# Kernel optimization log

Hardware: AMD Instinct MI355X
Metric: run time of the kernel (lower is better)

Reference implementation:

```python
import jax, jax.numpy as jnp
import numpy as np

HIDDEN = 1024
HEADS = 16
HEAD = HIDDEN // HEADS
EXPAND = 4096
EPS = 1e-5


def layer_norm(x, g, b):
    mu = jnp.mean(x, axis=-1, keepdims=True)
    var = jnp.mean((x - mu) ** 2, axis=-1, keepdims=True)
    return (x - mu) * jax.lax.rsqrt(var + EPS) * g + b


def setup_inputs() -> dict:
    key = jax.random.key(0)
    ks = jax.random.split(key, 12)
    s = 0.02
    return {
        "x": jax.random.normal(ks[0], (4, 2048, HIDDEN), dtype=jnp.float32),
        "Wqkv": jax.random.normal(ks[1], (HIDDEN, 3 * HIDDEN), dtype=jnp.float32) * s,
        "bqkv": jnp.zeros((3 * HIDDEN,), jnp.float32),
        "Wproj": jax.random.normal(ks[2], (HIDDEN, HIDDEN), dtype=jnp.float32) * s,
        "bproj": jnp.zeros((HIDDEN,), jnp.float32),
        "W1": jax.random.normal(ks[3], (HIDDEN, EXPAND), dtype=jnp.float32) * s,
        "b1": jnp.zeros((EXPAND,), jnp.float32),
        "W2": jax.random.normal(ks[4], (EXPAND, HIDDEN), dtype=jnp.float32) * s,
        "b2": jnp.zeros((HIDDEN,), jnp.float32),
        "g1": jnp.ones((HIDDEN,), jnp.float32),
        "be1": jnp.zeros((HIDDEN,), jnp.float32),
        "g2": jnp.ones((HIDDEN,), jnp.float32),
        "be2": jnp.zeros((HIDDEN,), jnp.float32),
    }


def attention(x, Wqkv, bqkv, Wproj, bproj):
    B, L, _ = x.shape
    qkv = (x @ Wqkv + bqkv).reshape(B, L, 3, HEADS, HEAD)
    q, k, v = [qkv[:, :, i].transpose(0, 2, 1, 3) for i in range(3)]  # [B,H,L,D]
    attn = jnp.einsum("bnld,bnkd->bnlk", q, k) / np.sqrt(HEAD).astype(np.float32)
    attn = jax.nn.softmax(attn, axis=-1)
    o = jnp.einsum("bnlk,bnkd->bnld", attn, v)
    o = o.transpose(0, 2, 1, 3).reshape(B, L, HIDDEN)
    return o @ Wproj + bproj


def reference(x, Wqkv, bqkv, Wproj, bproj, W1, b1, W2, b2, g1, be1, g2, be2):
    # post-norm transformer block (pre_norm=False), dropout=0 (eval)
    h = layer_norm(x + attention(x, Wqkv, bqkv, Wproj, bproj), g1, be1)
    ff = jax.nn.gelu(h @ W1 + b1, approximate=False) @ W2 + b2
    return layer_norm(h + ff, g2, be2)
```

## Files before the change

### kernel.cpp

```cpp
#include <hip/hip_runtime.h>
#include <hip/hip_bf16.h>
#include <math.h>


typedef __bf16 bf16_t;
typedef __bf16 bf16x8 __attribute__((ext_vector_type(8)));
typedef __bf16 bf16x4 __attribute__((ext_vector_type(4)));
typedef float f32x4 __attribute__((ext_vector_type(4)));
typedef float f32x16 __attribute__((ext_vector_type(16)));

#define HID   1024
#define NHEAD 16
#define HD    64
#define EXPD  4096
#define LSEQ  2048
#define BATCH 4
#define MROWS (BATCH * LSEQ)

#if __has_builtin(__builtin_amdgcn_exp2f)
#define EXP2F __builtin_amdgcn_exp2f
#else
#define EXP2F exp2f
#endif

__device__ __forceinline__ void gld_lds16(const bf16_t* g, bf16_t* l) {
  __builtin_amdgcn_global_load_lds(
      (const __attribute__((address_space(1))) void*)g,
      (__attribute__((address_space(3))) void*)l, 16, 0, 0);
}

__device__ __forceinline__ void vmwait(int n) {
  if (n == 8)      asm volatile("s_waitcnt vmcnt(8)" ::: "memory");
  else if (n == 4) asm volatile("s_waitcnt vmcnt(4)" ::: "memory");
  else if (n == 3) asm volatile("s_waitcnt vmcnt(3)" ::: "memory");
  else if (n == 0) asm volatile("s_waitcnt vmcnt(0)" ::: "memory");
}

__device__ __forceinline__ void block_bar() {
  asm volatile("" ::: "memory");
  __builtin_amdgcn_s_barrier();
  asm volatile("" ::: "memory");
}

__device__ __forceinline__ void swap32(unsigned& a, unsigned& b) {
#if __has_builtin(__builtin_amdgcn_permlane32_swap)
  auto r = __builtin_amdgcn_permlane32_swap(a, b, false, false);
  a = r[0]; b = r[1];
#else
  bool hiL = ((threadIdx.x & 63) >= 32);
  unsigned pa = (unsigned)__shfl_xor((int)a, 32, 64);
  unsigned pb = (unsigned)__shfl_xor((int)b, 32, 64);
  unsigned na = hiL ? pb : a;
  unsigned nb = hiL ? b : pa;
  a = na; b = nb;
#endif
}

__device__ __forceinline__ unsigned pk_bf16(float lo, float hi) {
  bf16_t l = (bf16_t)lo, h = (bf16_t)hi;
  unsigned short ul, uh;
  __builtin_memcpy(&ul, &l, 2);
  __builtin_memcpy(&uh, &h, 2);
  return (unsigned)ul | ((unsigned)uh << 16);
}

__device__ __forceinline__ float gelu_t(float v) {
  float u = v * (0.7978845608028654f + 0.0356774081f * v * v);
  float e = EXP2F(u * 2.885390082f);
  float th = (e - 1.f) / (e + 1.f);
  return 0.5f * v * (1.f + th);
}

__global__ __launch_bounds__(256) void cvt_bf16(const float* __restrict__ in,
                                                bf16_t* __restrict__ out, int n4) {
  int i = blockIdx.x * 256 + threadIdx.x;
  if (i >= n4) return;
  float4 v = ((const float4*)in)[i];
  bf16x4 o;
  o[0] = (bf16_t)v.x; o[1] = (bf16_t)v.y; o[2] = (bf16_t)v.z; o[3] = (bf16_t)v.w;
  ((bf16x4*)out)[i] = o;
}

__global__ __launch_bounds__(256) void transpose_cvt(const float* __restrict__ W,
                                                     bf16_t* __restrict__ Wt,
                                                     int K, int N) {
  __shared__ float tile[32][33];
  int n0 = blockIdx.x * 32, k0 = blockIdx.y * 32;
  int tx = threadIdx.x & 31, ty = threadIdx.x >> 5;
#pragma unroll
  for (int i = 0; i < 32; i += 8)
    tile[ty + i][tx] = W[(size_t)(k0 + ty + i) * N + n0 + tx];
  __syncthreads();
#pragma unroll
  for (int i = 0; i < 32; i += 8)
    Wt[(size_t)(n0 + ty + i) * K + k0 + tx] = (bf16_t)tile[tx][ty + i];
}

template <int BM, int BN, int NTHR>
__global__ __launch_bounds__(NTHR, (NTHR == 512 ? 4 : 3))
void gemm_k(const bf16_t* __restrict__ A,
            const bf16_t* __restrict__ Bt,
            const float* __restrict__ bias,
            void* __restrict__ C,
            float* __restrict__ C2,
            bf16_t* __restrict__ vTo,
            int M, int N, int K, int mode) {
  constexpr int WC = (NTHR / 64) / 2;
  constexpr int AL = BM * 4 / NTHR;
  constexpr int BL = BN * 4 / NTHR;
  constexpr int LOADS = AL + BL;
  constexpr int RSTEP = NTHR >> 2;
  __shared__ bf16_t smem[3 * BM * 32 + 3 * BN * 32];
  bf16_t* As = smem;
  bf16_t* Bs = smem + 3 * BM * 32;

  const int nbx = gridDim.x;
  int p = blockIdx.y * nbx + blockIdx.x;
  const int GM = 8;
  int group = p / (GM * nbx);
  int idx = p - group * (GM * nbx);
  const int by = group * GM + (idx & (GM - 1));
  const int bx = idx >> 3;
  const int n0 = bx * BN, m0 = by * BM;

  const int zz = blockIdx.z;
  const int kLen = K / (int)gridDim.z;
  const int kOff = zz * kLen;

  const int t = threadIdx.x;
  const int lane = t & 63, w = t >> 6;
  const int wr = w / WC, wc = w % WC;
  const int quad = lane >> 4, l16 = lane & 15;

  f32x4 acc[4][4];
#pragma unroll
  for (int i = 0; i < 4; ++i)
#pragma unroll
    for (int j = 0; j < 4; ++j) acc[i][j] = (f32x4){0.f, 0.f, 0.f, 0.f};

  const int r0 = t >> 2;
  const unsigned ksw = (((unsigned)t & 3u) ^ ((unsigned)(r0 >> 1) & 3u)) * 8u;
  const unsigned offR0 = (unsigned)r0 * (unsigned)K + ksw;

  const bf16_t* aB = A + (size_t)m0 * K + kOff;
  const bf16_t* bB = Bt + (size_t)n0 * K + kOff;

  unsigned aoff[4], boff[4];
#pragma unroll
  for (int i = 0; i < 4; ++i) {
    int row = wr * 64 + 16 * i + l16;
    aoff[i] = (unsigned)(row * 32 + (quad ^ ((row >> 1) & 3)) * 8);
  }
#pragma unroll
  for (int j = 0; j < 4; ++j) {
    int row = wc * 64 + 16 * j + l16;
    boff[j] = (unsigned)(row * 32 + (quad ^ ((row >> 1) & 3)) * 8);
  }

  auto stage = [&](int slot, int kk) {
    bf16_t* Asl = As + slot * (BM * 32);
    bf16_t* Bsl = Bs + slot * (BN * 32);
    const bf16_t* aS = aB + kk;
    const bf16_t* bS = bB + kk;
#pragma unroll
    for (int a = 0; a < AL; ++a)
      gld_lds16(aS + offR0 + (size_t)a * RSTEP * K, Asl + (t + a * NTHR) * 8);
#pragma unroll
    for (int b = 0; b < BL; ++b)
      gld_lds16(bS + offR0 + (size_t)b * RSTEP * K, Bsl + (t + b * NTHR) * 8);
  };

  const int NT = kLen >> 5;

  stage(0, 0);
  stage(1, 32);
  vmwait(LOADS);
  block_bar();

  int cs = 0;
  for (int kt = 0; kt < NT; ++kt) {
    if (kt < NT - 2) {
      int ss = cs == 0 ? 2 : cs - 1;
      stage(ss, (kt + 2) * 32);
    }
    const bf16_t* Asl = As + cs * (BM * 32);
    const bf16_t* Bsl = Bs + cs * (BN * 32);
    bf16x8 af[4], bfr[4];
#pragma unroll
    for (int i = 0; i < 4; ++i) af[i] = *(const bf16x8*)(Asl + aoff[i]);
#pragma unroll
    for (int j = 0; j < 4; ++j) bfr[j] = *(const bf16x8*)(Bsl + boff[j]);
    __builtin_amdgcn_s_setprio(1);
#pragma unroll
    for (int i = 0; i < 4; ++i)
#pragma unroll
      for (int j = 0; j < 4; ++j)
        acc[i][j] = __builtin_amdgcn_mfma_f32_16x16x32_bf16(af[i], bfr[j], acc[i][j], 0, 0, 0);
    __builtin_amdgcn_s_setprio(0);
    if (kt < NT - 2)      vmwait(LOADS);
    else if (kt == NT - 2) vmwait(0);
    if (kt < NT - 1) block_bar();
    cs = cs == 2 ? 0 : cs + 1;
  }

  if constexpr (BN == 256) {
    if (vTo != nullptr && n0 >= 2048) {
      const int bb = m0 >> 11;
      const int l0b = m0 & 2047;
      block_bar();
      bf16_t* T = smem;
#pragma unroll
      for (int i = 0; i < 4; ++i) {
        int rl = wr * 64 + 16 * i + quad * 4;
#pragma unroll
        for (int j = 0; j < 4; ++j) {
          int c = wc * 64 + 16 * j + l16;
          float bv = bias[n0 + c];
          bf16x4 pk;
#pragma unroll
          for (int r = 0; r < 4; ++r) pk[r] = (bf16_t)(acc[i][j][r] + bv);
          *(bf16x4*)(T + c * 132 + rl) = pk;
        }
      }
      block_bar();
      const int vbase = n0 - 2048;
#pragma unroll
      for (int s = 0; s < 4096 / NTHR; ++s) {
        int id = t + s * NTHR;
        int c = id >> 4, ch = id & 15;
        int hh = (vbase + c) >> 6, dd = (vbase + c) & 63;
        bf16x8 v8 = *(const bf16x8*)(T + c * 132 + ch * 8);
        *(bf16x8*)(vTo + ((size_t)((bb * 16 + hh) * 64 + dd)) * 2048 + l0b + ch * 8) = v8;
      }
      return;
    }
  }

#pragma unroll
  for (int i = 0; i < 4; ++i) {
    int rowb = m0 + wr * 64 + 16 * i + quad * 4;
#pragma unroll
    for (int j = 0; j < 4; ++j) {
      int col = n0 + wc * 64 + 16 * j + l16;
      float bv = (zz == 0) ? bias[col] : 0.f;
#pragma unroll
      for (int r = 0; r < 4; ++r) {
        float v = acc[i][j][r] + bv;
        size_t idx = (size_t)(rowb + r) * N + col;
        if (zz != 0) {
          C2[idx] = v;
        } else if (mode == 0) {
          ((bf16_t*)C)[idx] = (bf16_t)v;
        } else if (mode == 1) {
          ((bf16_t*)C)[idx] = (bf16_t)gelu_t(v);
        } else {
          ((float*)C)[idx] = v;
        }
      }
    }
  }
}

__global__ __launch_bounds__(512, 2)
void gemm_8x(const bf16_t* __restrict__ A,
             const bf16_t* __restrict__ Bt,
             const float* __restrict__ bias,
             bf16_t* __restrict__ C,
             int M, int N, int K) {
  __shared__ bf16_t smem[65536];
  const int nbx = gridDim.x;
  int p = blockIdx.y * nbx + blockIdx.x;
  const int GM = 8;
  int group = p / (GM * nbx);
  int idx = p - group * (GM * nbx);
  const int by = group * GM + (idx & (GM - 1));
  const int bx = idx >> 3;
  const int n0 = bx * 256, m0 = by * 256;

  const int t = threadIdx.x;
  const int lane = t & 63, w = t >> 6;
  const int wr = w >> 2, wc = w & 3;
  const int quad = lane >> 4, l16 = lane & 15;

  f32x4 acc[8][4];
#pragma unroll
  for (int i = 0; i < 8; ++i)
#pragma unroll
    for (int j = 0; j < 4; ++j) acc[i][j] = (f32x4){0.f, 0.f, 0.f, 0.f};

  const int r0 = t >> 2;
  const unsigned ksw = (((unsigned)t & 3u) ^ ((unsigned)(r0 >> 1) & 3u)) * 8u;
  const unsigned offR = (unsigned)r0 * (unsigned)K + ksw;

  const bf16_t* aB = A + (size_t)m0 * K;
  const bf16_t* bB = Bt + (size_t)n0 * K;

  unsigned aoff[8], boff[4];
#pragma unroll
  for (int i = 0; i < 8; ++i) {
    int row = wr * 128 + 16 * i + l16;
    aoff[i] = (unsigned)(row * 32 + (quad ^ ((row >> 1) & 3)) * 8);
  }
#pragma unroll
  for (int j = 0; j < 4; ++j) {
    int row = wc * 64 + 16 * j + l16;
    boff[j] = (unsigned)(16384 + row * 32 + (quad ^ ((row >> 1) & 3)) * 8);
  }

  auto stageChunk = [&](const bf16_t* src, int kk, int regionElem) {
    bf16_t* d = smem + regionElem;
    gld_lds16(src + kk + offR, d + t * 8);
    gld_lds16(src + kk + offR + (size_t)128 * K, d + t * 8 + 4096);
  };

  const int NT = K >> 6;

  stageChunk(aB, 0, 0);
  stageChunk(bB, 0, 16384);
  stageChunk(aB, 32, 8192);
  stageChunk(bB, 32, 24576);
  vmwait(4);
  block_bar();

  for (int kt = 0; kt < NT; ++kt) {
    const int sb = (kt & 1) * 32768;
    const int ss = ((kt + 1) & 1) * 32768;
    const int ktk = (kt + 1) * 64;
    const bool st = (kt + 1 < NT);
    bf16x8 af[8], b0, b1;
#pragma unroll
    for (int i = 0; i < 8; ++i) af[i] = *(const bf16x8*)(smem + sb + aoff[i]);
    b0 = *(const bf16x8*)(smem + sb + boff[0]);
    b1 = *(const bf16x8*)(smem + sb + boff[1]);
    if (st) stageChunk(aB, ktk, ss);
    __builtin_amdgcn_s_setprio(1);
#pragma unroll
    for (int i = 0; i < 8; ++i) {
      acc[i][0] = __builtin_amdgcn_mfma_f32_16x16x32_bf16(af[i], b0, acc[i][0], 0, 0, 0);
      acc[i][1] = __builtin_amdgcn_mfma_f32_16x16x32_bf16(af[i], b1, acc[i][1], 0, 0, 0);
    }
    __builtin_amdgcn_s_setprio(0);
    b0 = *(const bf16x8*)(smem + sb + boff[2]);
    b1 = *(const bf16x8*)(smem + sb + boff[3]);
    if (st) stageChunk(bB, ktk, ss + 16384);
    __builtin_amdgcn_s_setprio(1);
#pragma unroll
    for (int i = 0; i < 8; ++i) {
      acc[i][2] = __builtin_amdgcn_mfma_f32_16x16x32_bf16(af[i], b0, acc[i][2], 0, 0, 0);
      acc[i][3] = __builtin_amdgcn_mfma_f32_16x16x32_bf16(af[i], b1, acc[i][3], 0, 0, 0);
    }
    __builtin_amdgcn_s_setprio(0);
    if (st) vmwait(4); else vmwait(0);
    block_bar();
#pragma unroll
    for (int i = 0; i < 8; ++i) af[i] = *(const bf16x8*)(smem + sb + 8192 + aoff[i]);
    b0 = *(const bf16x8*)(smem + sb + 8192 + boff[0]);
    b1 = *(const bf16x8*)(smem + sb + 8192 + boff[1]);
    if (st) stageChunk(aB, ktk + 32, ss + 8192);
    __builtin_amdgcn_s_setprio(1);
#pragma unroll
    for (int i = 0; i < 8; ++i) {
      acc[i][0] = __builtin_amdgcn_mfma_f32_16x16x32_bf16(af[i], b0, acc[i][0], 0, 0, 0);
      acc[i][1] = __builtin_amdgcn_mfma_f32_16x16x32_bf16(af[i], b1, acc[i][1], 0, 0, 0);
    }
    __builtin_amdgcn_s_setprio(0);
    b0 = *(const bf16x8*)(smem + sb + 8192 + boff[2]);
    b1 = *(const bf16x8*)(smem + sb + 8192 + boff[3]);
    if (st) stageChunk(bB, ktk + 32, ss + 24576);
    __builtin_amdgcn_s_setprio(1);
#pragma unroll
    for (int i = 0; i < 8; ++i) {
      acc[i][2] = __builtin_amdgcn_mfma_f32_16x16x32_bf16(af[i], b0, acc[i][2], 0, 0, 0);
      acc[i][3] = __builtin_amdgcn_mfma_f32_16x16x32_bf16(af[i], b1, acc[i][3], 0, 0, 0);
    }
    __builtin_amdgcn_s_setprio(0);
    if (st) {
      vmwait(4);
      block_bar();
    }
  }

#pragma unroll
  for (int i = 0; i < 8; ++i) {
    int rowb = m0 + wr * 128 + 16 * i + quad * 4;
#pragma unroll
    for (int j = 0; j < 4; ++j) {
      int col = n0 + wc * 64 + 16 * j + l16;
      float bv = bias[col];
#pragma unroll
      for (int r = 0; r < 4; ++r) {
        float v = acc[i][j][r] + bv;
        C[(size_t)(rowb + r) * N + col] = (bf16_t)gelu_t(v);
      }
    }
  }
}

__global__ __launch_bounds__(256, 3) void attn_kernel(const bf16_t* __restrict__ qkv,
                                                      const bf16_t* __restrict__ vT,
                                                      bf16_t* __restrict__ ob) {
  __shared__ bf16_t smem[24576];
  bf16_t* Qs = smem + 16384;
  const int qt = blockIdx.x, h = blockIdx.y, b = blockIdx.z;
  const int t = threadIdx.x, lane = t & 63, w = t >> 6;
  const int l32 = lane & 31, hi = lane >> 5;
  const size_t RS = 3 * HID;
  const int bh = b * NHEAD + h;

  const bf16_t* qbase = qkv + ((size_t)(b * LSEQ + qt * 128)) * RS + h * HD;
  const bf16_t* kbase = qkv + ((size_t)b * LSEQ) * RS + HID + h * HD;
  const bf16_t* vtbase = vT + (size_t)bh * HD * LSEQ;

#pragma unroll
  for (int s = 0; s < 4; ++s) {
    int l = t + s * 256;
    int r = l >> 3, c8 = l & 7;
    gld_lds16(qbase + (size_t)r * RS + ((c8 ^ (r & 7)) * 8), Qs + l * 8);
  }
  __syncthreads();

  const float sc = 0.18033688011112042f;
  bf16x8 bq[4];
  {
    int qrow = 32 * w + l32;
#pragma unroll
    for (int c = 0; c < 4; ++c) {
      int y = 2 * c + hi;
      bf16x8 q8 = *(const bf16x8*)(Qs + qrow * 64 + ((y ^ (qrow & 7)) * 8));
#pragma unroll
      for (int e = 0; e < 8; ++e) q8[e] = (bf16_t)((float)q8[e] * sc);
      bq[c] = q8;
    }
  }

  bf16x8 ones8;
#pragma unroll
  for (int e = 0; e < 8; ++e) ones8[e] = (bf16_t)1.0f;

  auto stageKV = [&](int slot, int kt) {
    bf16_t* Ks = smem + slot * 8192;
    bf16_t* Vts = Ks + 4096;
#pragma unroll
    for (int s = 0; s < 2; ++s) {
      int l = t + s * 256;
      int r = l >> 3, c8 = l & 7;
      gld_lds16(kbase + (size_t)(kt * 64 + r) * RS + ((c8 ^ (r & 7)) * 8), Ks + l * 8);
      gld_lds16(vtbase + (size_t)r * LSEQ + kt * 64 + ((c8 ^ (r & 7)) * 8), Vts + l * 8);
    }
  };

  f32x16 accO[2], accS;
#pragma unroll
  for (int dt = 0; dt < 2; ++dt)
#pragma unroll
    for (int e = 0; e < 16; ++e) accO[dt][e] = 0.f;
#pragma unroll
  for (int e = 0; e < 16; ++e) accS[e] = 0.f;

  constexpr int NT = LSEQ / 64;
  stageKV(0, 0);

  for (int kt = 0; kt < NT; ++kt) {
    const int cs = kt & 1;
    if (kt + 1 < NT) {
      stageKV(1 - cs, kt + 1);
      vmwait(4);
    } else {
      vmwait(0);
    }
    block_bar();
    const bf16_t* Ks = smem + cs * 8192;
    const bf16_t* Vts = Ks + 4096;

    f32x16 s0, s1;
#pragma unroll
    for (int e = 0; e < 16; ++e) { s0[e] = 0.f; s1[e] = 0.f; }
    __builtin_amdgcn_s_setprio(1);
#pragma unroll
    for (int c = 0; c < 4; ++c) {
      int y = 2 * c + hi;
      int r0 = l32;
      bf16x8 a0 = *(const bf16x8*)(Ks + r0 * 64 + ((y ^ (r0 & 7)) * 8));
      s0 = __builtin_amdgcn_mfma_f32_32x32x16_bf16(a0, bq[c], s0, 0, 0, 0);
      int r1 = 32 + l32;
      bf16x8 a1 = *(const bf16x8*)(Ks + r1 * 64 + ((y ^ (r1 & 7)) * 8));
      s1 = __builtin_amdgcn_mfma_f32_32x32x16_bf16(a1, bq[c], s1, 0, 0, 0);
    }
    __builtin_amdgcn_s_setprio(0);

    unsigned pf[2][2][4];
#pragma unroll
    for (int stile = 0; stile < 2; ++stile) {
      f32x16& sv = stile ? s1 : s0;
      float p[16];
#pragma unroll
      for (int e = 0; e < 16; ++e) p[e] = EXP2F(sv[e]);
      unsigned lo[4], hi_[4];
#pragma unroll
      for (int g = 0; g < 4; ++g) {
        lo[g] = pk_bf16(p[4 * g + 0], p[4 * g + 1]);
        hi_[g] = pk_bf16(p[4 * g + 2], p[4 * g + 3]);
      }
#pragma unroll
      for (int c2 = 0; c2 < 2; ++c2) {
        unsigned aL = lo[2 * c2], bL = lo[2 * c2 + 1];
        swap32(aL, bL);
        pf[stile][c2][0] = aL; pf[stile][c2][2] = bL;
        unsigned aH = hi_[2 * c2], bH = hi_[2 * c2 + 1];
        swap32(aH, bH);
        pf[stile][c2][1] = aH; pf[stile][c2][3] = bH;
      }
    }

    __builtin_amdgcn_s_setprio(1);
#pragma unroll
    for (int dt = 0; dt < 2; ++dt)
#pragma unroll
      for (int stile = 0; stile < 2; ++stile)
#pragma unroll
        for (int c2 = 0; c2 < 2; ++c2) {
          int c8v = stile * 4 + c2 * 2 + hi;
          int rv = dt * 32 + l32;
          bf16x8 av = *(const bf16x8*)(Vts + rv * 64 + ((c8v ^ (rv & 7)) * 8));
          union { unsigned u[4]; bf16x8 v; } bp;
          bp.u[0] = pf[stile][c2][0]; bp.u[1] = pf[stile][c2][1];
          bp.u[2] = pf[stile][c2][2]; bp.u[3] = pf[stile][c2][3];
          accO[dt] = __builtin_amdgcn_mfma_f32_32x32x16_bf16(av, bp.v, accO[dt], 0, 0, 0);
        }
#pragma unroll
    for (int stile = 0; stile < 2; ++stile)
#pragma unroll
      for (int c2 = 0; c2 < 2; ++c2) {
        union { unsigned u[4]; bf16x8 v; } bp;
        bp.u[0] = pf[stile][c2][0]; bp.u[1] = pf[stile][c2][1];
        bp.u[2] = pf[stile][c2][2]; bp.u[3] = pf[stile][c2][3];
        accS = __builtin_amdgcn_mfma_f32_32x32x16_bf16(ones8, bp.v, accS, 0, 0, 0);
      }
    __builtin_amdgcn_s_setprio(0);
    block_bar();
  }

  float inv = 1.f / accS[0];

  bf16_t* Osh = smem;
  {
    int q = 32 * w + l32;
#pragma unroll
    for (int dt = 0; dt < 2; ++dt)
#pragma unroll
      for (int e = 0; e < 16; ++e) {
        int d = dt * 32 + (e & 3) + 8 * (e >> 2) + 4 * hi;
        Osh[q * 68 + d] = (bf16_t)(accO[dt][e] * inv);
      }
  }
  __syncthreads();
#pragma unroll
  for (int s = 0; s < 4; ++s) {
    int l = t + s * 256;
    int r = l >> 3, c8 = l & 7;
    bf16x8 v = *(const bf16x8*)(Osh + r * 68 + c8 * 8);
    *(bf16x8*)(ob + ((size_t)(b * LSEQ + qt * 128 + r)) * HID + h * HD + c8 * 8) = v;
  }
}

__global__ __launch_bounds__(256) void resid_ln(const float* __restrict__ X,
                                                const float* __restrict__ Y,
                                                const float* __restrict__ Y2,
                                                const float* __restrict__ g,
                                                const float* __restrict__ be,
                                                float* __restrict__ outf,
                                                bf16_t* __restrict__ outb) {
  const int row = blockIdx.x;
  const int t = threadIdx.x;
  float4 a = ((const float4*)X)[(size_t)row * 256 + t];
  float4 bvec = ((const float4*)Y)[(size_t)row * 256 + t];
  float4 cvec = {0.f, 0.f, 0.f, 0.f};
  if (Y2) cvec = ((const float4*)Y2)[(size_t)row * 256 + t];
  float v0 = a.x + bvec.x + cvec.x, v1 = a.y + bvec.y + cvec.y;
  float v2 = a.z + bvec.z + cvec.z, v3 = a.w + bvec.w + cvec.w;
  float s = v0 + v1 + v2 + v3;
  float s2 = v0 * v0 + v1 * v1 + v2 * v2 + v3 * v3;
#pragma unroll
  for (int msk = 1; msk < 64; msk <<= 1) {
    s += __shfl_xor(s, msk, 64);
    s2 += __shfl_xor(s2, msk, 64);
  }
  __shared__ float red[8];
  int w = t >> 6;
  if ((t & 63) == 0) { red[w] = s; red[w + 4] = s2; }
  __syncthreads();
  s = red[0] + red[1] + red[2] + red[3];
  s2 = red[4] + red[5] + red[6] + red[7];
  float mu = s * (1.f / 1024.f);
  float var = s2 * (1.f / 1024.f) - mu * mu;
  float rstd = rsqrtf(var + 1e-5f);
  float4 gg = ((const float4*)g)[t];
  float4 bb = ((const float4*)be)[t];
  float o0 = (v0 - mu) * rstd * gg.x + bb.x;
  float o1 = (v1 - mu) * rstd * gg.y + bb.y;
  float o2 = (v2 - mu) * rstd * gg.z + bb.z;
  float o3 = (v3 - mu) * rstd * gg.w + bb.w;
  float4 o = {o0, o1, o2, o3};
  ((float4*)outf)[(size_t)row * 256 + t] = o;
  if (outb) {
    bf16x4 ob4;
    ob4[0] = (bf16_t)o0; ob4[1] = (bf16_t)o1; ob4[2] = (bf16_t)o2; ob4[3] = (bf16_t)o3;
    ((bf16x4*)outb)[(size_t)row * 256 + t] = ob4;
  }
}

extern "C" void kernel_launch(void* const* d_in, const int* in_sizes, int n_in,
                              void* d_out, int out_size, void* d_ws, size_t ws_size,
                              hipStream_t stream) {
  const float* x     = (const float*)d_in[0];
  const float* Wqkv  = (const float*)d_in[1];
  const float* bqkv  = (const float*)d_in[2];
  const float* Wproj = (const float*)d_in[3];
  const float* bproj = (const float*)d_in[4];
  const float* W1    = (const float*)d_in[5];
  const float* b1    = (const float*)d_in[6];
  const float* W2    = (const float*)d_in[7];
  const float* b2    = (const float*)d_in[8];
  const float* g1    = (const float*)d_in[9];
  const float* be1   = (const float*)d_in[10];
  const float* g2    = (const float*)d_in[11];
  const float* be2   = (const float*)d_in[12];
  float* out = (float*)d_out;

  char* ws = (char*)d_ws;
  bf16_t* w2T    = (bf16_t*)(ws);
  float*  h      = (float*) (ws + ((size_t)8 << 20));
  float*  a_f2   = (float*) (ws + ((size_t)40 << 20));
  bf16_t* qkv_ff = (bf16_t*)(ws + ((size_t)72 << 20));
  char*   E      = ws + ((size_t)136 << 20);
  bf16_t* wqkvT  = (bf16_t*)(E);
  bf16_t* wprojT = (bf16_t*)(E + ((size_t)6 << 20));
  bf16_t* w1T    = (bf16_t*)(E + ((size_t)8 << 20));
  char*   xb_ob  = E + ((size_t)16 << 20);
  bf16_t* hb     = (bf16_t*)(E + ((size_t)32 << 20));
  float*  f2b    = (float*)E;

  bf16_t* xb    = (bf16_t*)xb_ob;
  bf16_t* ob    = (bf16_t*)xb_ob;
  bf16_t* qkvb  = qkv_ff;
  bf16_t* ff1b  = qkv_ff;
  float*  attnf = a_f2;
  float*  ff2f  = a_f2;
  bf16_t* vTg   = hb;

  dim3 blk(256);
  dim3 blk512(512);
  transpose_cvt<<<dim3(3072 / 32, 1024 / 32), blk, 0, stream>>>(Wqkv, wqkvT, 1024, 3072);
  transpose_cvt<<<dim3(1024 / 32, 1024 / 32), blk, 0, stream>>>(Wproj, wprojT, 1024, 1024);
  transpose_cvt<<<dim3(4096 / 32, 1024 / 32), blk, 0, stream>>>(W1, w1T, 1024, 4096);
  transpose_cvt<<<dim3(1024 / 32, 4096 / 32), blk, 0, stream>>>(W2, w2T, 4096, 1024);
  cvt_bf16<<<MROWS * HID / 4 / 256, blk, 0, stream>>>(x, xb, MROWS * HID / 4);

  gemm_k<128, 256, 512><<<dim3(3072 / 256, MROWS / 128), blk512, 0, stream>>>(
      xb, wqkvT, bqkv, qkvb, nullptr, vTg, MROWS, 3072, 1024, 0);
  attn_kernel<<<dim3(LSEQ / 128, NHEAD, BATCH), blk, 0, stream>>>(qkvb, vTg, ob);
  gemm_k<128, 256, 512><<<dim3(1024 / 256, MROWS / 128, 2), blk512, 0, stream>>>(
      ob, wprojT, bproj, attnf, h, nullptr, MROWS, 1024, 1024, 2);
  resid_ln<<<MROWS, blk, 0, stream>>>(x, attnf, h, g1, be1, h, hb);
  gemm_8x<<<dim3(4096 / 256, MROWS / 256), blk512, 0, stream>>>(
      hb, w1T, b1, ff1b, MROWS, 4096, 1024);
  gemm_k<128, 256, 512><<<dim3(1024 / 256, MROWS / 128, 2), blk512, 0, stream>>>(
      ff1b, w2T, b2, ff2f, f2b, nullptr, MROWS, 1024, 4096, 2);
  resid_ln<<<MROWS, blk, 0, stream>>>(h, ff2f, f2b, g2, be2, out, (bf16_t*)nullptr);
}
```

Before: 532.0 us.

## Double attention query tile per block to reuse K/V tiles across more queries

The attention kernel now processes 256 query rows per block instead of 128, with each wave handling two 32-row query sub-tiles. Each K/V tile staged in shared memory and each K/V fragment read from LDS is reused for twice as many MFMAs, which halves global K/V traffic and the barrier count per query. In exchange it uses more registers and LDS, drops occupancy to 2 blocks per CU, and halves the grid to 512 blocks.

```diff
diff --git a/kernel.cpp b/kernel.cpp
--- a/kernel.cpp
+++ b/kernel.cpp
@@ -396,10 +396,10 @@
   }
 }
 
-__global__ __launch_bounds__(256, 3) void attn_kernel(const bf16_t* __restrict__ qkv,
+__global__ __launch_bounds__(256, 2) void attn_kernel(const bf16_t* __restrict__ qkv,
                                                       const bf16_t* __restrict__ vT,
                                                       bf16_t* __restrict__ ob) {
-  __shared__ bf16_t smem[24576];
+  __shared__ bf16_t smem[32768];
   bf16_t* Qs = smem + 16384;
   const int qt = blockIdx.x, h = blockIdx.y, b = blockIdx.z;
   const int t = threadIdx.x, lane = t & 63, w = t >> 6;
@@ -407,12 +407,12 @@
   const size_t RS = 3 * HID;
   const int bh = b * NHEAD + h;
 
-  const bf16_t* qbase = qkv + ((size_t)(b * LSEQ + qt * 128)) * RS + h * HD;
+  const bf16_t* qbase = qkv + ((size_t)(b * LSEQ + qt * 256)) * RS + h * HD;
   const bf16_t* kbase = qkv + ((size_t)b * LSEQ) * RS + HID + h * HD;
   const bf16_t* vtbase = vT + (size_t)bh * HD * LSEQ;
 
 #pragma unroll
-  for (int s = 0; s < 4; ++s) {
+  for (int s = 0; s < 8; ++s) {
     int l = t + s * 256;
     int r = l >> 3, c8 = l & 7;
     gld_lds16(qbase + (size_t)r * RS + ((c8 ^ (r & 7)) * 8), Qs + l * 8);
@@ -420,16 +420,21 @@
   __syncthreads();
 
   const float sc = 0.18033688011112042f;
-  bf16x8 bq[4];
+  bf16x8 bqA[4], bqB[4];
   {
-    int qrow = 32 * w + l32;
+    int qA = 64 * w + l32, qB = qA + 32;
 #pragma unroll
     for (int c = 0; c < 4; ++c) {
       int y = 2 * c + hi;
-      bf16x8 q8 = *(const bf16x8*)(Qs + qrow * 64 + ((y ^ (qrow & 7)) * 8));
-#pragma unroll
-      for (int e = 0; e < 8; ++e) q8[e] = (bf16_t)((float)q8[e] * sc);
-      bq[c] = q8;
+      bf16x8 qa = *(const bf16x8*)(Qs + qA * 64 + ((y ^ (qA & 7)) * 8));
+      bf16x8 qb = *(const bf16x8*)(Qs + qB * 64 + ((y ^ (qB & 7)) * 8));
+#pragma unroll
+      for (int e = 0; e < 8; ++e) {
+        qa[e] = (bf16_t)((float)qa[e] * sc);
+        qb[e] = (bf16_t)((float)qb[e] * sc);
+      }
+      bqA[c] = qa;
+      bqB[c] = qb;
     }
   }
 
@@ -449,13 +454,13 @@
     }
   };
 
-  f32x16 accO[2], accS;
-#pragma unroll
-  for (int dt = 0; dt < 2; ++dt)
-#pragma unroll
-    for (int e = 0; e < 16; ++e) accO[dt][e] = 0.f;
-#pragma unroll
-  for (int e = 0; e < 16; ++e) accS[e] = 0.f;
+  f32x16 accOA[2], accOB[2], accSA, accSB, z16;
+#pragma unroll
+  for (int e = 0; e < 16; ++e) {
+    accOA[0][e] = 0.f; accOA[1][e] = 0.f;
+    accOB[0][e] = 0.f; accOB[1][e] = 0.f;
+    accSA[e] = 0.f; accSB[e] = 0.f; z16[e] = 0.f;
+  }
 
   constexpr int NT = LSEQ / 64;
   stageKV(0, 0);
@@ -472,45 +477,58 @@
     const bf16_t* Ks = smem + cs * 8192;
     const bf16_t* Vts = Ks + 4096;
 
-    f32x16 s0, s1;
-#pragma unroll
-    for (int e = 0; e < 16; ++e) { s0[e] = 0.f; s1[e] = 0.f; }
+    f32x16 sA0, sA1, sB0, sB1;
     __builtin_amdgcn_s_setprio(1);
-#pragma unroll
-    for (int c = 0; c < 4; ++c) {
+    {
+      int y = hi;
+      int r0 = l32, r1 = 32 + l32;
+      bf16x8 a0 = *(const bf16x8*)(Ks + r0 * 64 + ((y ^ (r0 & 7)) * 8));
+      bf16x8 a1 = *(const bf16x8*)(Ks + r1 * 64 + ((y ^ (r1 & 7)) * 8));
+      sA0 = __builtin_amdgcn_mfma_f32_32x32x16_bf16(a0, bqA[0], z16, 0, 0, 0);
+      sA1 = __builtin_amdgcn_mfma_f32_32x32x16_bf16(a1, bqA[0], z16, 0, 0, 0);
+      sB0 = __builtin_amdgcn_mfma_f32_32x32x16_bf16(a0, bqB[0], z16, 0, 0, 0);
+      sB1 = __builtin_amdgcn_mfma_f32_32x32x16_bf16(a1, bqB[0], z16, 0, 0, 0);
+    }
+#pragma unroll
+    for (int c = 1; c < 4; ++c) {
       int y = 2 * c + hi;
-      int r0 = l32;
+      int r0 = l32, r1 = 32 + l32;
       bf16x8 a0 = *(const bf16x8*)(Ks + r0 * 64 + ((y ^ (r0 & 7)) * 8));
-      s0 = __builtin_amdgcn_mfma_f32_32x32x16_bf16(a0, bq[c], s0, 0, 0, 0);
-      int r1 = 32 + l32;
       bf16x8 a1 = *(const bf16x8*)(Ks + r1 * 64 + ((y ^ (r1 & 7)) * 8));
-      s1 = __builtin_amdgcn_mfma_f32_32x32x16_bf16(a1, bq[c], s1, 0, 0, 0);
+      sA0 = __builtin_amdgcn_mfma_f32_32x32x16_bf16(a0, bqA[c], sA0, 0, 0, 0);
+      sA1 = __builtin_amdgcn_mfma_f32_32x32x16_bf16(a1, bqA[c], sA1, 0, 0, 0);
+      sB0 = __builtin_amdgcn_mfma_f32_32x32x16_bf16(a0, bqB[c], sB0, 0, 0, 0);
+      sB1 = __builtin_amdgcn_mfma_f32_32x32x16_bf16(a1, bqB[c], sB1, 0, 0, 0);
     }
     __builtin_amdgcn_s_setprio(0);
 
-    unsigned pf[2][2][4];
-#pragma unroll
-    for (int stile = 0; stile < 2; ++stile) {
-      f32x16& sv = stile ? s1 : s0;
-      float p[16];
-#pragma unroll
-      for (int e = 0; e < 16; ++e) p[e] = EXP2F(sv[e]);
-      unsigned lo[4], hi_[4];
-#pragma unroll
-      for (int g = 0; g < 4; ++g) {
-        lo[g] = pk_bf16(p[4 * g + 0], p[4 * g + 1]);
-        hi_[g] = pk_bf16(p[4 * g + 2], p[4 * g + 3]);
-      }
-#pragma unroll
-      for (int c2 = 0; c2 < 2; ++c2) {
-        unsigned aL = lo[2 * c2], bL = lo[2 * c2 + 1];
-        swap32(aL, bL);
-        pf[stile][c2][0] = aL; pf[stile][c2][2] = bL;
-        unsigned aH = hi_[2 * c2], bH = hi_[2 * c2 + 1];
-        swap32(aH, bH);
-        pf[stile][c2][1] = aH; pf[stile][c2][3] = bH;
-      }
-    }
+    unsigned pfA[2][2][4], pfB[2][2][4];
+    auto mkpf = [&](f32x16& s0, f32x16& s1, unsigned (&pf)[2][2][4]) {
+#pragma unroll
+      for (int stile = 0; stile < 2; ++stile) {
+        f32x16& sv = stile ? s1 : s0;
+        float p[16];
+#pragma unroll
+        for (int e = 0; e < 16; ++e) p[e] = EXP2F(sv[e]);
+        unsigned lo[4], hi_[4];
+#pragma unroll
+        for (int g = 0; g < 4; ++g) {
+          lo[g] = pk_bf16(p[4 * g + 0], p[4 * g + 1]);
+          hi_[g] = pk_bf16(p[4 * g + 2], p[4 * g + 3]);
+        }
+#pragma unroll
+        for (int c2 = 0; c2 < 2; ++c2) {
+          unsigned aL = lo[2 * c2], bL = lo[2 * c2 + 1];
+          swap32(aL, bL);
+          pf[stile][c2][0] = aL; pf[stile][c2][2] = bL;
+          unsigned aH = hi_[2 * c2], bH = hi_[2 * c2 + 1];
+          swap32(aH, bH);
+          pf[stile][c2][1] = aH; pf[stile][c2][3] = bH;
+        }
+      }
+    };
+    mkpf(sA0, sA1, pfA);
+    mkpf(sB0, sB1, pfB);
 
     __builtin_amdgcn_s_setprio(1);
 #pragma unroll
@@ -522,44 +540,52 @@
           int c8v = stile * 4 + c2 * 2 + hi;
           int rv = dt * 32 + l32;
           bf16x8 av = *(const bf16x8*)(Vts + rv * 64 + ((c8v ^ (rv & 7)) * 8));
-          union { unsigned u[4]; bf16x8 v; } bp;
-          bp.u[0] = pf[stile][c2][0]; bp.u[1] = pf[stile][c2][1];
-          bp.u[2] = pf[stile][c2][2]; bp.u[3] = pf[stile][c2][3];
-          accO[dt] = __builtin_amdgcn_mfma_f32_32x32x16_bf16(av, bp.v, accO[dt], 0, 0, 0);
+          union { unsigned u[4]; bf16x8 v; } ba, bb;
+          ba.u[0] = pfA[stile][c2][0]; ba.u[1] = pfA[stile][c2][1];
+          ba.u[2] = pfA[stile][c2][2]; ba.u[3] = pfA[stile][c2][3];
+          bb.u[0] = pfB[stile][c2][0]; bb.u[1] = pfB[stile][c2][1];
+          bb.u[2] = pfB[stile][c2][2]; bb.u[3] = pfB[stile][c2][3];
+          accOA[dt] = __builtin_amdgcn_mfma_f32_32x32x16_bf16(av, ba.v, accOA[dt], 0, 0, 0);
+          accOB[dt] = __builtin_amdgcn_mfma_f32_32x32x16_bf16(av, bb.v, accOB[dt], 0, 0, 0);
         }
 #pragma unroll
     for (int stile = 0; stile < 2; ++stile)
 #pragma unroll
       for (int c2 = 0; c2 < 2; ++c2) {
-        union { unsigned u[4]; bf16x8 v; } bp;
-        bp.u[0] = pf[stile][c2][0]; bp.u[1] = pf[stile][c2][1];
-        bp.u[2] = pf[stile][c2][2]; bp.u[3] = pf[stile][c2][3];
-        accS = __builtin_amdgcn_mfma_f32_32x32x16_bf16(ones8, bp.v, accS, 0, 0, 0);
+        union { unsigned u[4]; bf16x8 v; } ba, bb;
+        ba.u[0] = pfA[stile][c2][0]; ba.u[1] = pfA[stile][c2][1];
+        ba.u[2] = pfA[stile][c2][2]; ba.u[3] = pfA[stile][c2][3];
+        bb.u[0] = pfB[stile][c2][0]; bb.u[1] = pfB[stile][c2][1];
+        bb.u[2] = pfB[stile][c2][2]; bb.u[3] = pfB[stile][c2][3];
+        accSA = __builtin_amdgcn_mfma_f32_32x32x16_bf16(ones8, ba.v, accSA, 0, 0, 0);
+        accSB = __builtin_amdgcn_mfma_f32_32x32x16_bf16(ones8, bb.v, accSB, 0, 0, 0);
       }
     __builtin_amdgcn_s_setprio(0);
     block_bar();
   }
 
-  float inv = 1.f / accS[0];
+  float invA = 1.f / accSA[0];
+  float invB = 1.f / accSB[0];
 
   bf16_t* Osh = smem;
   {
-    int q = 32 * w + l32;
+    int qA = 64 * w + l32, qB = qA + 32;
 #pragma unroll
     for (int dt = 0; dt < 2; ++dt)
 #pragma unroll
       for (int e = 0; e < 16; ++e) {
         int d = dt * 32 + (e & 3) + 8 * (e >> 2) + 4 * hi;
-        Osh[q * 68 + d] = (bf16_t)(accO[dt][e] * inv);
+        Osh[qA * 68 + d] = (bf16_t)(accOA[dt][e] * invA);
+        Osh[qB * 68 + d] = (bf16_t)(accOB[dt][e] * invB);
       }
   }
   __syncthreads();
 #pragma unroll
-  for (int s = 0; s < 4; ++s) {
+  for (int s = 0; s < 8; ++s) {
     int l = t + s * 256;
     int r = l >> 3, c8 = l & 7;
     bf16x8 v = *(const bf16x8*)(Osh + r * 68 + c8 * 8);
-    *(bf16x8*)(ob + ((size_t)(b * LSEQ + qt * 128 + r)) * HID + h * HD + c8 * 8) = v;
+    *(bf16x8*)(ob + ((size_t)(b * LSEQ + qt * 256 + r)) * HID + h * HD + c8 * 8) = v;
   }
 }
 
@@ -658,7 +684,7 @@
 
   gemm_k<128, 256, 512><<<dim3(3072 / 256, MROWS / 128), blk512, 0, stream>>>(
       xb, wqkvT, bqkv, qkvb, nullptr, vTg, MROWS, 3072, 1024, 0);
-  attn_kernel<<<dim3(LSEQ / 128, NHEAD, BATCH), blk, 0, stream>>>(qkvb, vTg, ob);
+  attn_kernel<<<dim3(LSEQ / 256, NHEAD, BATCH), blk, 0, stream>>>(qkvb, vTg, ob);
   gemm_k<128, 256, 512><<<dim3(1024 / 256, MROWS / 128, 2), blk512, 0, stream>>>(
       ob, wprojT, bproj, attnf, h, nullptr, MROWS, 1024, 1024, 2);
   resid_ln<<<MROWS, blk, 0, stream>>>(x, attnf, h, g1, be1, h, hb);
```

Result: faster. 515.2 us (-3.2%).
